# Kernel tuning notes

Hardware: AMD Instinct MI355X
Metric: run time of the kernel (lower is better)

The kernel has to match this reference:

```python
import jax, jax.numpy as jnp
import numpy as np

B, C, H, W = 32, 256, 56, 56
NH, WS, SS = 8, 7, 3
N = WS * WS
EPS = 1e-5


def _rel_pos_index(ws):
    ch, cw = np.meshgrid(np.arange(ws), np.arange(ws), indexing='ij')
    coords = np.stack([ch.reshape(-1), cw.reshape(-1)])  # (2, N)
    rel = coords[:, :, None] - coords[:, None, :]        # (2, N, N)
    rel = rel.transpose(1, 2, 0)
    rel[:, :, 0] += ws - 1
    rel[:, :, 1] += ws - 1
    rel[:, :, 0] *= 2 * ws - 1
    return rel.sum(-1)  # (N, N) int


def _attn_mask(Hh, Ww, ws, ss):
    img = np.zeros((Hh, Ww), dtype=np.float32)
    cnt = 0
    for hs in (slice(0, -ws), slice(-ws, -ss), slice(-ss, None)):
        for wsl in (slice(0, -ws), slice(-ws, -ss), slice(-ss, None)):
            img[hs, wsl] = cnt
            cnt += 1
    mw = img.reshape(Hh // ws, ws, Ww // ws, ws).transpose(0, 2, 1, 3).reshape(-1, ws * ws)
    am = mw[:, None, :] - mw[:, :, None]
    return np.where(am != 0, np.float32(-100.0), np.float32(0.0))  # (nW, N, N)

RPI = _rel_pos_index(WS)
AMASK = _attn_mask(H, W, WS, SS)


def _ln(x, w, b):
    mu = x.mean(-1, keepdims=True)
    var = ((x - mu) ** 2).mean(-1, keepdims=True)
    return (x - mu) * jax.lax.rsqrt(var + EPS) * w + b


def setup_inputs() -> dict:
    key = jax.random.key(0)
    ks = jax.random.split(key, 10)
    s = 0.02
    return {
        'x': jax.random.normal(ks[0], (B, C, H, W), jnp.float32),
        'qkv_w': jax.random.normal(ks[1], (3 * C, C), jnp.float32) * s,
        'q_bias': jnp.zeros((C,), jnp.float32),
        'v_bias': jnp.zeros((C,), jnp.float32),
        'proj_w': jax.random.normal(ks[2], (C, C), jnp.float32) * s,
        'proj_b': jnp.zeros((C,), jnp.float32),
        'rpb_table': jax.random.normal(ks[3], ((2 * WS - 1) * (2 * WS - 1), NH), jnp.float32) * s,
        'norm1_w': jnp.ones((C,), jnp.float32),
        'norm1_b': jnp.zeros((C,), jnp.float32),
        'norm2_w': jnp.ones((C,), jnp.float32),
        'norm2_b': jnp.zeros((C,), jnp.float32),
        'fc1_w': jax.random.normal(ks[4], (4 * C, C), jnp.float32) * s,
        'fc1_b': jnp.zeros((4 * C,), jnp.float32),
        'fc2_w': jax.random.normal(ks[5], (C, 4 * C), jnp.float32) * s,
        'fc2_b': jnp.zeros((C,), jnp.float32),
    }


def reference(x, qkv_w, q_bias, v_bias, proj_w, proj_b, rpb_table,
              norm1_w, norm1_b, norm2_w, norm2_b, fc1_w, fc1_b, fc2_w, fc2_b):
    b = x.shape[0]
    hd = C // NH
    scale = hd ** -0.5
    nWh, nWw = H // WS, W // WS
    nW = nWh * nWw

    # (B,C,H,W) -> (B, L, C)
    xs = x.transpose(0, 2, 3, 1).reshape(b, H * W, C)
    shortcut = xs
    xn = _ln(xs, norm1_w, norm1_b).reshape(b, H, W, C)
    # cyclic shift
    xn = jnp.roll(xn, (-SS, -SS), axis=(1, 2))
    # window partition -> (B*nW, N, C)
    xw = xn.reshape(b, nWh, WS, nWw, WS, C).transpose(0, 1, 3, 2, 4, 5).reshape(b * nW, N, C)

    qkv_bias = jnp.concatenate([q_bias, jnp.zeros_like(v_bias), v_bias])
    qkv = xw @ qkv_w.T + qkv_bias                      # (B_, N, 3C)
    qkv = qkv.reshape(b * nW, N, 3, NH, hd).transpose(2, 0, 3, 1, 4)
    q, k, v = qkv[0], qkv[1], qkv[2]                   # (B_, NH, N, hd)

    attn = jnp.einsum('whnd,whmd->whnm', q * scale, k)  # (B_, NH, N, N)
    bias = rpb_table[RPI.reshape(-1)].reshape(N, N, NH).transpose(2, 0, 1)
    attn = attn + bias[None]
    attn = attn.reshape(b, nW, NH, N, N) + jnp.asarray(AMASK)[None, :, None]
    attn = jax.nn.softmax(attn.reshape(b * nW, NH, N, N), axis=-1)

    out = jnp.einsum('whnm,whmd->whnd', attn, v)        # (B_, NH, N, hd)
    out = out.transpose(0, 2, 1, 3).reshape(b * nW, N, C)
    out = out @ proj_w.T + proj_b

    # window reverse + un-shift
    out = out.reshape(b, nWh, nWw, WS, WS, C).transpose(0, 1, 3, 2, 4, 5).reshape(b, H, W, C)
    out = jnp.roll(out, (SS, SS), axis=(1, 2)).reshape(b, H * W, C)

    xs = shortcut + out
    h = _ln(xs, norm2_w, norm2_b)
    h = jax.nn.relu(h @ fc1_w.T + fc1_b) @ fc2_w.T + fc2_b
    xs = xs + h
    return xs.reshape(b, H, W, C).transpose(0, 3, 1, 2)
```

## Files before the change

kernel.cpp:

```cpp
#include <hip/hip_runtime.h>
#include <math.h>

#define EPS 1e-5f

constexpr int Bc = 32, Cc = 256, Hc = 56, Wc = 56;
constexpr int NHc = 8, HDc = 32, WSc = 7, SSc = 3;
constexpr int NTOK = 49;
constexpr int NWIN = 64;
constexpr int Lc = Hc * Wc;
constexpr int Mrows = Bc * NWIN * NTOK;
constexpr int GIMG = 8;
constexpr int NGRP = Bc / GIMG;
constexpr int ROWS_G = GIMG * Lc;
constexpr int WIN_G = GIMG * NWIN;

typedef short bf16x8 __attribute__((ext_vector_type(8)));
typedef float f32x4 __attribute__((ext_vector_type(4)));
typedef unsigned short u16x8 __attribute__((ext_vector_type(8)));
typedef unsigned short u16x4 __attribute__((ext_vector_type(4)));

__device__ __forceinline__ float bf2f(unsigned short u) {
    return __uint_as_float(((unsigned)u) << 16);
}
__device__ __forceinline__ unsigned short f2bf(float f) {
    unsigned x = __float_as_uint(f);
    return (unsigned short)((x + 0x7fffu + ((x >> 16) & 1u)) >> 16);
}
__device__ __forceinline__ void gload_lds16(const void* g, void* l) {
    __builtin_amdgcn_global_load_lds(
        (const __attribute__((address_space(1))) unsigned int*)g,
        (__attribute__((address_space(3))) unsigned int*)l, 16, 0, 0);
}
__device__ __forceinline__ void inv_swz(int bp, int& row, int& ch) {
    int b2 = ((bp >> 2) ^ (bp >> 4)) & 1;
    int b1_ = ((bp >> 1) ^ (bp >> 3)) & 1;
    int b0 = (bp ^ (bp >> 2) ^ (bp >> 4)) & 1;
    int B = (bp & ~7) | (b2 << 2) | (b1_ << 1) | b0;
    row = B >> 2; ch = B & 3;
}

__global__ __launch_bounds__(256) void k_prep(const float* __restrict__ qkv_w,
                                              const float* __restrict__ proj_w,
                                              const float* __restrict__ w1,
                                              const float* __restrict__ w2,
                                              const float* __restrict__ qb,
                                              const float* __restrict__ vb,
                                              unsigned short* __restrict__ qkv_wb,
                                              unsigned short* __restrict__ proj_wb,
                                              unsigned short* __restrict__ w1t,
                                              unsigned short* __restrict__ w2t,
                                              float* __restrict__ qkvb) {
    int i = blockIdx.x * 256 + threadIdx.x;
    if (i < 768) qkvb[i] = (i < 256) ? qb[i] : ((i < 512) ? 0.f : vb[i - 512]);
    if (i < 196608) qkv_wb[i] = f2bf(qkv_w[i]);
    if (i < 65536)  proj_wb[i] = f2bf(proj_w[i]);
    if (i < 262144) {
        int n1 = i >> 8, k1 = i & 255;
        w1t[((n1 >> 4) * 32 + (k1 >> 3)) * 128 + (n1 & 15) * 8 + (k1 & 7)] = f2bf(w1[i]);
        int n2 = i >> 10, k2 = i & 1023;
        w2t[((k2 >> 6) * 32 + (n2 >> 4) * 2 + ((k2 >> 5) & 1)) * 512 +
            ((k2 >> 3) & 3) * 128 + (n2 & 15) * 8 + (k2 & 7)] = f2bf(w2[i]);
    }
}

__global__ __launch_bounds__(256) void k_ln1_part(const float* __restrict__ x,
                                                  const float* __restrict__ n1w,
                                                  const float* __restrict__ n1b,
                                                  unsigned short* __restrict__ xw,
                                                  unsigned short* __restrict__ xres,
                                                  int b0) {
    __shared__ float s[Cc * 57];
    __shared__ float mu[Wc], rs[Wc];
    int bg = blockIdx.x / Hc, h = blockIdx.x % Hc;
    int b = b0 + bg;
    int t = threadIdx.x;
    const float* xp = x + ((size_t)b * Cc) * Lc + h * Wc;
    for (int idx = t; idx < Cc * Wc; idx += 256) {
        int c = idx / Wc, w = idx % Wc;
        s[c * 57 + w] = xp[(size_t)c * Lc + w];
    }
    __syncthreads();
    int lane = t & 63, wv = t >> 6;
    for (int p = wv; p < Wc; p += 4) {
        float sum = 0.f, sq = 0.f;
        #pragma unroll
        for (int k = 0; k < 4; ++k) {
            float v = s[(lane + 64 * k) * 57 + p];
            sum += v; sq += v * v;
        }
        #pragma unroll
        for (int off = 32; off; off >>= 1) {
            sum += __shfl_xor(sum, off);
            sq  += __shfl_xor(sq, off);
        }
        if (lane == 0) {
            float m = sum / Cc;
            mu[p] = m;
            rs[p] = rsqrtf(sq / Cc - m * m + EPS);
        }
    }
    __syncthreads();
    float wc_ = n1w[t], bc_ = n1b[t];
    int hr = (h + Hc - SSc) % Hc;
    int whh = hr / WSc, th = hr % WSc;
    for (int p = 0; p < Wc; ++p) {
        float raw = s[t * 57 + p];
        xres[((size_t)bg * Lc + h * Wc + p) * Cc + t] = f2bf(raw);
        int wr = (p + Wc - SSc) % Wc;
        int www = wr / WSc, tw = wr % WSc;
        int row = (b * NWIN + whh * 8 + www) * NTOK + th * WSc + tw;
        float v = (raw - mu[p]) * rs[p] * wc_ + bc_;
        xw[(size_t)row * Cc + t] = f2bf(v);
    }
}

__global__ __launch_bounds__(256) void k_gemm_mfma(const unsigned short* __restrict__ A,
                                                   const unsigned short* __restrict__ W,
                                                   const float* __restrict__ bias,
                                                   unsigned short* __restrict__ outb,
                                                   int K, int Nd) {
    __shared__ unsigned short As[128 * 32];
    __shared__ unsigned short Bs[128 * 32];
    int t = threadIdx.x;
    int l = t & 63, w = t >> 6;
    int wm = w & 1, wn = w >> 1;
    int m0 = blockIdx.x * 128, n0 = blockIdx.y * 128;
    int lr = l & 15, lg = l >> 4;

    int row0, ch0, row1, ch1;
    inv_swz(w * 128 + l, row0, ch0);
    inv_swz(w * 128 + 64 + l, row1, ch1);
    const unsigned short* gA0 = A + (size_t)(m0 + row0) * K + ch0 * 8;
    const unsigned short* gA1 = A + (size_t)(m0 + row1) * K + ch1 * 8;
    const unsigned short* gB0 = W + (size_t)(n0 + row0) * K + ch0 * 8;
    const unsigned short* gB1 = W + (size_t)(n0 + row1) * K + ch1 * 8;
    unsigned short* lA0 = &As[(w * 128) * 8];
    unsigned short* lA1 = &As[(w * 128 + 64) * 8];
    unsigned short* lB0 = &Bs[(w * 128) * 8];
    unsigned short* lB1 = &Bs[(w * 128 + 64) * 8];

    f32x4 acc[4][4];
    #pragma unroll
    for (int i = 0; i < 4; ++i)
        #pragma unroll
        for (int j = 0; j < 4; ++j)
            acc[i][j] = (f32x4){0.f, 0.f, 0.f, 0.f};

    for (int kt = 0; kt < K; kt += 32) {
        gload_lds16(gA0 + kt, lA0);
        gload_lds16(gA1 + kt, lA1);
        gload_lds16(gB0 + kt, lB0);
        gload_lds16(gB1 + kt, lB1);
        __syncthreads();
        bf16x8 af[4], bfr[4];
        #pragma unroll
        for (int i = 0; i < 4; ++i) {
            int ra = wm * 64 + i * 16 + lr;
            af[i] = *(bf16x8*)&As[(ra * 32 + lg * 8) ^ ((ra & 7) << 3)];
            int rb = wn * 64 + i * 16 + lr;
            bfr[i] = *(bf16x8*)&Bs[(rb * 32 + lg * 8) ^ ((rb & 7) << 3)];
        }
        #pragma unroll
        for (int i = 0; i < 4; ++i)
            #pragma unroll
            for (int j = 0; j < 4; ++j)
                acc[i][j] = __builtin_amdgcn_mfma_f32_16x16x32_bf16(af[i], bfr[j], acc[i][j], 0, 0, 0);
        __syncthreads();
    }

    float bj[4];
    #pragma unroll
    for (int j = 0; j < 4; ++j) bj[j] = bias[n0 + wn * 64 + j * 16 + lr];
    #pragma unroll
    for (int i = 0; i < 4; ++i)
        #pragma unroll
        for (int j = 0; j < 4; ++j) {
            int col = n0 + wn * 64 + j * 16 + lr;
            #pragma unroll
            for (int r = 0; r < 4; ++r) {
                int row = m0 + wm * 64 + i * 16 + lg * 4 + r;
                outb[(size_t)row * Nd + col] = f2bf(acc[i][j][r] + bj[j]);
            }
        }
}

__global__ __launch_bounds__(256) void k_gemm_proj(const unsigned short* __restrict__ A,
                                                   const unsigned short* __restrict__ W,
                                                   const float* __restrict__ bias,
                                                   const unsigned short* __restrict__ xres,
                                                   unsigned short* __restrict__ xs) {
    __shared__ unsigned short As[128 * 32];
    __shared__ unsigned short Bs[128 * 32];
    constexpr int K = 256;
    int t = threadIdx.x;
    int l = t & 63, w = t >> 6;
    int wm = w & 1, wn = w >> 1;
    int m0 = blockIdx.x * 128, n0 = blockIdx.y * 128;
    int lr = l & 15, lg = l >> 4;

    int row0, ch0, row1, ch1;
    inv_swz(w * 128 + l, row0, ch0);
    inv_swz(w * 128 + 64 + l, row1, ch1);
    const unsigned short* gA0 = A + (size_t)(m0 + row0) * K + ch0 * 8;
    const unsigned short* gA1 = A + (size_t)(m0 + row1) * K + ch1 * 8;
    const unsigned short* gB0 = W + (size_t)(n0 + row0) * K + ch0 * 8;
    const unsigned short* gB1 = W + (size_t)(n0 + row1) * K + ch1 * 8;
    unsigned short* lA0 = &As[(w * 128) * 8];
    unsigned short* lA1 = &As[(w * 128 + 64) * 8];
    unsigned short* lB0 = &Bs[(w * 128) * 8];
    unsigned short* lB1 = &Bs[(w * 128 + 64) * 8];

    f32x4 acc[4][4];
    #pragma unroll
    for (int i = 0; i < 4; ++i)
        #pragma unroll
        for (int j = 0; j < 4; ++j)
            acc[i][j] = (f32x4){0.f, 0.f, 0.f, 0.f};

    for (int kt = 0; kt < K; kt += 32) {
        gload_lds16(gA0 + kt, lA0);
        gload_lds16(gA1 + kt, lA1);
        gload_lds16(gB0 + kt, lB0);
        gload_lds16(gB1 + kt, lB1);
        __syncthreads();
        bf16x8 af[4], bfr[4];
        #pragma unroll
        for (int i = 0; i < 4; ++i) {
            int ra = wm * 64 + i * 16 + lr;
            af[i] = *(bf16x8*)&As[(ra * 32 + lg * 8) ^ ((ra & 7) << 3)];
            int rb = wn * 64 + i * 16 + lr;
            bfr[i] = *(bf16x8*)&Bs[(rb * 32 + lg * 8) ^ ((rb & 7) << 3)];
        }
        #pragma unroll
        for (int i = 0; i < 4; ++i)
            #pragma unroll
            for (int j = 0; j < 4; ++j)
                acc[i][j] = __builtin_amdgcn_mfma_f32_16x16x32_bf16(af[i], bfr[j], acc[i][j], 0, 0, 0);
        __syncthreads();
    }

    float bj[4];
    #pragma unroll
    for (int j = 0; j < 4; ++j) bj[j] = bias[n0 + wn * 64 + j * 16 + lr];
    #pragma unroll
    for (int i = 0; i < 4; ++i)
        #pragma unroll
        for (int j = 0; j < 4; ++j) {
            int col = n0 + wn * 64 + j * 16 + lr;
            #pragma unroll
            for (int r = 0; r < 4; ++r) {
                int row = m0 + wm * 64 + i * 16 + lg * 4 + r;
                int wl = row / NTOK, tok = row - wl * NTOK;
                int bg = wl >> 6, wi = wl & 63;
                int hr = (wi >> 3) * 7 + tok / 7;
                int wr = (wi & 7) * 7 + tok % 7;
                int hh = hr + SSc; if (hh >= Hc) hh -= Hc;
                int ww = wr + SSc; if (ww >= Wc) ww -= Wc;
                size_t didx = ((size_t)bg * Lc + hh * Wc + ww) * Cc + col;
                float res = bf2f(xres[didx]);
                xs[didx] = f2bf(res + acc[i][j][r] + bj[j]);
            }
        }
}

__global__ __launch_bounds__(256) void k_attn(const unsigned short* __restrict__ qkv,
                                              const float* __restrict__ rpb,
                                              unsigned short* __restrict__ outb) {
    __shared__ unsigned short lds[4 * 6144 + 1352];
    unsigned short* rpbs = &lds[4 * 6144];
    int t = threadIdx.x;
    int w = t >> 6, l = t & 63;
    int lr = l & 15, lg = l >> 4;
    unsigned short* wl = &lds[w * 6144];
    unsigned short* Qs = wl;
    unsigned short* Ks = wl + 2048;
    unsigned short* Pm = wl;
    unsigned short* Vt = wl + 4096;

    for (int i = t; i < 1352; i += 256) rpbs[i] = f2bf(rpb[i]);

    int gid = blockIdx.x * 4 + w;
    int b_ = gid >> 3, hh = gid & 7;
    const unsigned short* base = qkv + (size_t)b_ * NTOK * 768 + hh * HDc;

    {
        int j = l;
        u16x8 vq[4], vk[4], vv[4];
        if (j < NTOK) {
            const unsigned short* rp = base + j * 768;
            #pragma unroll
            for (int s = 0; s < 4; ++s) {
                vq[s] = *(const u16x8*)(rp + s * 8);
                vk[s] = *(const u16x8*)(rp + 256 + s * 8);
                vv[s] = *(const u16x8*)(rp + 512 + s * 8);
            }
        } else {
            u16x8 z = {0, 0, 0, 0, 0, 0, 0, 0};
            #pragma unroll
            for (int s = 0; s < 4; ++s) { vq[s] = z; vk[s] = z; vv[s] = z; }
        }
        #pragma unroll
        for (int s = 0; s < 4; ++s) {
            int off = (j * 32 + s * 8) ^ ((j & 7) << 3);
            *(u16x8*)&Qs[off] = vq[s];
            *(u16x8*)&Ks[off] = vk[s];
        }
        #pragma unroll
        for (int s = 0; s < 4; ++s)
            #pragma unroll
            for (int e = 0; e < 8; ++e) {
                int d = s * 8 + e;
                Vt[d * 64 + (j ^ ((d & 7) << 3))] = ((unsigned short*)&vv[s])[e];
            }
    }
    __syncthreads();

    bf16x8 aq[4], bk[4];
    #pragma unroll
    for (int mt = 0; mt < 4; ++mt) {
        int row = mt * 16 + lr;
        int off = (row * 32 + lg * 8) ^ ((row & 7) << 3);
        aq[mt] = *(bf16x8*)&Qs[off];
        bk[mt] = *(bf16x8*)&Ks[off];
    }
    f32x4 sc[4][4];
    #pragma unroll
    for (int mt = 0; mt < 4; ++mt)
        #pragma unroll
        for (int nt = 0; nt < 4; ++nt)
            sc[mt][nt] = __builtin_amdgcn_mfma_f32_16x16x32_bf16(
                aq[mt], bk[nt], (f32x4){0.f, 0.f, 0.f, 0.f}, 0, 0, 0);

    const float scale = 0.17677669529663687f;
    int wi = b_ & 63, wh = wi >> 3, wwc = wi & 7;
    int jh[4], jw[4], ridJ[4];
    #pragma unroll
    for (int nt = 0; nt < 4; ++nt) {
        int j = nt * 16 + lr;
        jh[nt] = j / 7; jw[nt] = j - jh[nt] * 7;
        int gh = wh * 7 + jh[nt], gw = wwc * 7 + jw[nt];
        int rh = gh < 49 ? 0 : (gh < 53 ? 1 : 2);
        int rw = gw < 49 ? 0 : (gw < 53 ? 1 : 2);
        ridJ[nt] = rh * 3 + rw;
    }

    float rowrcp[4][4];
    #pragma unroll
    for (int mt = 0; mt < 4; ++mt) {
        #pragma unroll
        for (int r = 0; r < 4; ++r) {
            int i = mt * 16 + lg * 4 + r;
            int ih = i / 7, iw = i - ih * 7;
            int gh = wh * 7 + ih, gw = wwc * 7 + iw;
            int rhI = gh < 49 ? 0 : (gh < 53 ? 1 : 2);
            int rwI = gw < 49 ? 0 : (gw < 53 ? 1 : 2);
            int ridI = rhI * 3 + rwI;
            bool ivalid = (i < NTOK);
            float vals[4];
            float vmax = -1e30f;
            #pragma unroll
            for (int nt = 0; nt < 4; ++nt) {
                int j = nt * 16 + lr;
                float v = -1e30f;
                if (ivalid && j < NTOK) {
                    int rpi = (ih - jh[nt] + 6) * 13 + (iw - jw[nt] + 6);
                    float bv = bf2f(rpbs[rpi * 8 + hh]);
                    float msk = (ridI == ridJ[nt]) ? 0.f : -100.f;
                    v = sc[mt][nt][r] * scale + bv + msk;
                }
                vals[nt] = v;
                vmax = fmaxf(vmax, v);
            }
            #pragma unroll
            for (int off = 1; off < 16; off <<= 1)
                vmax = fmaxf(vmax, __shfl_xor(vmax, off));
            float s = 0.f;
            unsigned short pb[4];
            #pragma unroll
            for (int nt = 0; nt < 4; ++nt) {
                float e = (vals[nt] > -1e29f) ? __expf(vals[nt] - vmax) : 0.f;
                s += e;
                pb[nt] = f2bf(e);
            }
            #pragma unroll
            for (int off = 1; off < 16; off <<= 1)
                s += __shfl_xor(s, off);
            rowrcp[mt][r] = 1.f / s;
            #pragma unroll
            for (int nt = 0; nt < 4; ++nt) {
                int j = nt * 16 + lr;
                Pm[(i * 64 + j) ^ ((i & 7) << 3)] = pb[nt];
            }
        }
    }

    f32x4 o[4][2];
    #pragma unroll
    for (int mt = 0; mt < 4; ++mt)
        #pragma unroll
        for (int nt = 0; nt < 2; ++nt)
            o[mt][nt] = (f32x4){0.f, 0.f, 0.f, 0.f};
    #pragma unroll
    for (int ks = 0; ks < 2; ++ks) {
        bf16x8 ap[4], bv2[2];
        #pragma unroll
        for (int mt = 0; mt < 4; ++mt) {
            int row = mt * 16 + lr;
            ap[mt] = *(bf16x8*)&Pm[(row * 64 + ks * 32 + lg * 8) ^ ((row & 7) << 3)];
        }
        #pragma unroll
        for (int nt = 0; nt < 2; ++nt) {
            int n = nt * 16 + lr;
            bv2[nt] = *(bf16x8*)&Vt[(n * 64 + ks * 32 + lg * 8) ^ ((n & 7) << 3)];
        }
        #pragma unroll
        for (int mt = 0; mt < 4; ++mt)
            #pragma unroll
            for (int nt = 0; nt < 2; ++nt)
                o[mt][nt] = __builtin_amdgcn_mfma_f32_16x16x32_bf16(ap[mt], bv2[nt], o[mt][nt], 0, 0, 0);
    }

    #pragma unroll
    for (int mt = 0; mt < 4; ++mt)
        #pragma unroll
        for (int r = 0; r < 4; ++r) {
            int i = mt * 16 + lg * 4 + r;
            if (i < NTOK) {
                float rc = rowrcp[mt][r];
                #pragma unroll
                for (int nt = 0; nt < 2; ++nt) {
                    int d = nt * 16 + lr;
                    outb[((size_t)b_ * NTOK + i) * Cc + hh * HDc + d] = f2bf(o[mt][nt][r] * rc);
                }
            }
        }
}

#define HIDX(m, c) (((m) * 64 + (c)) ^ (((m) & 7) << 3))
__global__ __launch_bounds__(512) void k_mlp_fused(const unsigned short* __restrict__ xs,
                                                   const float* __restrict__ n2w,
                                                   const float* __restrict__ n2b,
                                                   const unsigned short* __restrict__ w1t,
                                                   const float* __restrict__ b1,
                                                   const unsigned short* __restrict__ w2t,
                                                   const float* __restrict__ b2,
                                                   float* __restrict__ out) {
    __shared__ unsigned short w1s[16384];
    __shared__ unsigned short w2s[16384];
    __shared__ unsigned short hid[8192];
    int t = threadIdx.x;
    int l = t & 63, w = t >> 6;
    int wm = w >> 1, wn = w & 1;
    int lr = l & 15, lg = l >> 4;
    int m0 = blockIdx.x * 128;

    bf16x8 xf[2][8];
    {
        #pragma unroll
        for (int mf = 0; mf < 2; ++mf) {
            int row = m0 + wm * 32 + mf * 16 + lr;
            const unsigned short* xrow = xs + (size_t)row * Cc;
            u16x8 raw[8];
            float sum = 0.f, sq = 0.f;
            #pragma unroll
            for (int ks = 0; ks < 8; ++ks) {
                raw[ks] = *(const u16x8*)(xrow + ks * 32 + lg * 8);
                #pragma unroll
                for (int e = 0; e < 8; ++e) {
                    float f = bf2f(raw[ks][e]);
                    sum += f; sq += f * f;
                }
            }
            sum += __shfl_xor(sum, 16); sq += __shfl_xor(sq, 16);
            sum += __shfl_xor(sum, 32); sq += __shfl_xor(sq, 32);
            float mu = sum / Cc;
            float rsg = rsqrtf(sq / Cc - mu * mu + EPS);
            #pragma unroll
            for (int ks = 0; ks < 8; ++ks) {
                #pragma unroll
                for (int e = 0; e < 8; ++e) {
                    int c = ks * 32 + lg * 8 + e;
                    float nv = (bf2f(raw[ks][e]) - mu) * rsg * n2w[c] + n2b[c];
                    ((unsigned short*)&xf[mf][ks])[e] = f2bf(nv);
                }
            }
        }
    }

    f32x4 acc2[2][8];
    #pragma unroll
    for (int mf = 0; mf < 2; ++mf)
        #pragma unroll
        for (int nf = 0; nf < 8; ++nf)
            acc2[mf][nf] = (f32x4){0.f, 0.f, 0.f, 0.f};

    u16x8 p1[4], p2[4];
    #pragma unroll
    for (int i = 0; i < 4; ++i) {
        int idx = (i * 512 + t) * 8;
        p1[i] = *(const u16x8*)(w1t + idx);
        p2[i] = *(const u16x8*)(w2t + idx);
    }

    for (int ch = 0; ch < 16; ++ch) {
        #pragma unroll
        for (int i = 0; i < 4; ++i) {
            int idx = (i * 512 + t) * 8;
            *(u16x8*)&w1s[idx] = p1[i];
            *(u16x8*)&w2s[idx] = p2[i];
        }
        __syncthreads();
        if (ch < 15) {
            const unsigned short* n1 = w1t + (ch + 1) * 16384;
            const unsigned short* n2 = w2t + (ch + 1) * 16384;
            #pragma unroll
            for (int i = 0; i < 4; ++i) {
                int idx = (i * 512 + t) * 8;
                p1[i] = *(const u16x8*)(n1 + idx);
                p2[i] = *(const u16x8*)(n2 + idx);
            }
        }
        {
            f32x4 acc1[2][2];
            #pragma unroll
            for (int ht = 0; ht < 2; ++ht)
                #pragma unroll
                for (int mf = 0; mf < 2; ++mf)
                    acc1[ht][mf] = (f32x4){0.f, 0.f, 0.f, 0.f};
            #pragma unroll
            for (int ks = 0; ks < 8; ++ks) {
                bf16x8 wfr[2];
                #pragma unroll
                for (int ht = 0; ht < 2; ++ht)
                    wfr[ht] = *(const bf16x8*)&w1s[(wn * 2 + ht) * 4096 + ks * 512 + l * 8];
                #pragma unroll
                for (int ht = 0; ht < 2; ++ht) {
                    acc1[ht][0] = __builtin_amdgcn_mfma_f32_16x16x32_bf16(wfr[ht], xf[0][ks], acc1[ht][0], 0, 0, 0);
                    acc1[ht][1] = __builtin_amdgcn_mfma_f32_16x16x32_bf16(wfr[ht], xf[1][ks], acc1[ht][1], 0, 0, 0);
                }
            }
            #pragma unroll
            for (int ht = 0; ht < 2; ++ht) {
                float b1v[4];
                #pragma unroll
                for (int r = 0; r < 4; ++r)
                    b1v[r] = b1[ch * 64 + (wn * 2 + ht) * 16 + lg * 4 + r];
                #pragma unroll
                for (int mf = 0; mf < 2; ++mf) {
                    u16x4 pk;
                    #pragma unroll
                    for (int r = 0; r < 4; ++r)
                        pk[r] = f2bf(fmaxf(acc1[ht][mf][r] + b1v[r], 0.f));
                    int m = wm * 32 + mf * 16 + lr;
                    int off = m * 64 + ((((wn * 2 + ht) * 16) + lg * 4) ^ ((m & 7) << 3));
                    *(u16x4*)&hid[off] = pk;
                }
            }
        }
        __syncthreads();
        {
            bf16x8 a[2][2];
            #pragma unroll
            for (int mf = 0; mf < 2; ++mf)
                #pragma unroll
                for (int ks = 0; ks < 2; ++ks) {
                    int m = wm * 32 + mf * 16 + lr;
                    a[mf][ks] = *(const bf16x8*)&hid[HIDX(m, ks * 32 + lg * 8)];
                }
            #pragma unroll
            for (int ks = 0; ks < 2; ++ks)
                #pragma unroll
                for (int nf = 0; nf < 8; ++nf) {
                    int nt = (wn * 128 + nf * 16) >> 4;
                    bf16x8 bfr = *(const bf16x8*)&w2s[(nt * 2 + ks) * 512 + l * 8];
                    acc2[0][nf] = __builtin_amdgcn_mfma_f32_16x16x32_bf16(a[0][ks], bfr, acc2[0][nf], 0, 0, 0);
                    acc2[1][nf] = __builtin_amdgcn_mfma_f32_16x16x32_bf16(a[1][ks], bfr, acc2[1][nf], 0, 0, 0);
                }
        }
        __syncthreads();
    }

    int b0i = m0 / Lc, l0 = m0 % Lc;
    #pragma unroll
    for (int nf = 0; nf < 8; ++nf) {
        int c = wn * 128 + nf * 16 + lr;
        float b2c = b2[c];
        #pragma unroll
        for (int mf = 0; mf < 2; ++mf)
            #pragma unroll
            for (int r = 0; r < 4; ++r) {
                int m = wm * 32 + mf * 16 + lg * 4 + r;
                float res = bf2f(xs[(size_t)(m0 + m) * Cc + c]);
                int lm = l0 + m;
                int bi = b0i + (lm >= Lc);
                if (lm >= Lc) lm -= Lc;
                out[((size_t)bi * Cc + c) * Lc + lm] = acc2[mf][nf][r] + b2c + res;
            }
    }
}

extern "C" void kernel_launch(void* const* d_in, const int* in_sizes, int n_in,
                              void* d_out, int out_size, void* d_ws, size_t ws_size,
                              hipStream_t stream) {
    const float* x      = (const float*)d_in[0];
    const float* qkv_w  = (const float*)d_in[1];
    const float* q_bias = (const float*)d_in[2];
    const float* v_bias = (const float*)d_in[3];
    const float* proj_w = (const float*)d_in[4];
    const float* proj_b = (const float*)d_in[5];
    const float* rpb    = (const float*)d_in[6];
    const float* n1w    = (const float*)d_in[7];
    const float* n1b    = (const float*)d_in[8];
    const float* n2w    = (const float*)d_in[9];
    const float* n2b    = (const float*)d_in[10];
    const float* w1     = (const float*)d_in[11];
    const float* b1     = (const float*)d_in[12];
    const float* w2     = (const float*)d_in[13];
    const float* b2     = (const float*)d_in[14];

    char* ws = (char*)d_ws;
    const size_t SZ_BF16 = (size_t)Mrows * Cc * 2;
    unsigned short* xw      = (unsigned short*)ws;
    float*          qkvb    = (float*)(ws + SZ_BF16);
    unsigned short* qkv_wb  = (unsigned short*)(ws + SZ_BF16 + 3072);
    unsigned short* proj_wb = qkv_wb + 196608;
    unsigned short* w1t     = proj_wb + 65536;
    unsigned short* w2t     = w1t + 262144;

    unsigned short* qkv_s  = (unsigned short*)d_out;
    unsigned short* attn_s = qkv_s + (size_t)ROWS_G * 768;
    unsigned short* xres_s = attn_s + (size_t)ROWS_G * Cc;

    k_prep<<<1024, 256, 0, stream>>>(qkv_w, proj_w, w1, w2, q_bias, v_bias,
                                     qkv_wb, proj_wb, w1t, w2t, qkvb);

    for (int g = 0; g < NGRP; ++g) {
        unsigned short* xw_g = xw + (size_t)g * ROWS_G * Cc;
        k_ln1_part<<<GIMG * Hc, 256, 0, stream>>>(x, n1w, n1b, xw, xres_s, g * GIMG);
        k_gemm_mfma<<<dim3(ROWS_G / 128, 768 / 128), 256, 0, stream>>>(
            xw_g, qkv_wb, qkvb, qkv_s, 256, 768);
        k_attn<<<WIN_G * NHc / 4, 256, 0, stream>>>(qkv_s, rpb, attn_s);
        k_gemm_proj<<<dim3(ROWS_G / 128, 2), 256, 0, stream>>>(
            attn_s, proj_wb, proj_b, xres_s, xw_g);
    }

    k_mlp_fused<<<Mrows / 128, 512, 0, stream>>>(xw, n2w, n2b, w1t, b1, w2t, b2,
                                                 (float*)d_out);
}
```

Before: 567.2 us.

## Write attention output in place over qkv, double group size, stream fc2 weights

The attention kernel now writes its output in place into the Q slot of the qkv scratch buffer, and the projection GEMM reads A with a row stride of 768. This drops the separate attention buffer, so the d_out scratch can hold groups of 16 images instead of 8, halving the number of per-group launches. The fused MLP no longer stages fc2 weights in LDS and reads them straight from global/L2 per fragment. That cuts LDS use, which may improve occupancy, but adds global load latency inside the MFMA loop. The in-place write is safe only if each wave has finished reading its Q slice before writing, which holds because each (window, head) pair touches only its own Q columns.

```diff
diff --git a/kernel.cpp b/kernel.cpp
--- a/kernel.cpp
+++ b/kernel.cpp
@@ -9,7 +9,7 @@
 constexpr int NWIN = 64;
 constexpr int Lc = Hc * Wc;
 constexpr int Mrows = Bc * NWIN * NTOK;
-constexpr int GIMG = 8;
+constexpr int GIMG = 16;
 constexpr int NGRP = Bc / GIMG;
 constexpr int ROWS_G = GIMG * Lc;
 constexpr int WIN_G = GIMG * NWIN;
@@ -192,6 +192,7 @@
     __shared__ unsigned short As[128 * 32];
     __shared__ unsigned short Bs[128 * 32];
     constexpr int K = 256;
+    constexpr int LDA = 768;
     int t = threadIdx.x;
     int l = t & 63, w = t >> 6;
     int wm = w & 1, wn = w >> 1;
@@ -201,8 +202,8 @@
     int row0, ch0, row1, ch1;
     inv_swz(w * 128 + l, row0, ch0);
     inv_swz(w * 128 + 64 + l, row1, ch1);
-    const unsigned short* gA0 = A + (size_t)(m0 + row0) * K + ch0 * 8;
-    const unsigned short* gA1 = A + (size_t)(m0 + row1) * K + ch1 * 8;
+    const unsigned short* gA0 = A + (size_t)(m0 + row0) * LDA + ch0 * 8;
+    const unsigned short* gA1 = A + (size_t)(m0 + row1) * LDA + ch1 * 8;
     const unsigned short* gB0 = W + (size_t)(n0 + row0) * K + ch0 * 8;
     const unsigned short* gB1 = W + (size_t)(n0 + row1) * K + ch1 * 8;
     unsigned short* lA0 = &As[(w * 128) * 8];
@@ -263,9 +264,8 @@
         }
 }
 
-__global__ __launch_bounds__(256) void k_attn(const unsigned short* __restrict__ qkv,
-                                              const float* __restrict__ rpb,
-                                              unsigned short* __restrict__ outb) {
+__global__ __launch_bounds__(256) void k_attn(unsigned short* __restrict__ qkv,
+                                              const float* __restrict__ rpb) {
     __shared__ unsigned short lds[4 * 6144 + 1352];
     unsigned short* rpbs = &lds[4 * 6144];
     int t = threadIdx.x;
@@ -281,7 +281,7 @@
 
     int gid = blockIdx.x * 4 + w;
     int b_ = gid >> 3, hh = gid & 7;
-    const unsigned short* base = qkv + (size_t)b_ * NTOK * 768 + hh * HDc;
+    unsigned short* base = qkv + (size_t)b_ * NTOK * 768 + hh * HDc;
 
     {
         int j = l;
@@ -430,7 +430,7 @@
                 #pragma unroll
                 for (int nt = 0; nt < 2; ++nt) {
                     int d = nt * 16 + lr;
-                    outb[((size_t)b_ * NTOK + i) * Cc + hh * HDc + d] = f2bf(o[mt][nt][r] * rc);
+                    qkv[((size_t)b_ * NTOK + i) * 768 + hh * HDc + d] = f2bf(o[mt][nt][r] * rc);
                 }
             }
         }
@@ -446,7 +446,6 @@
                                                    const float* __restrict__ b2,
                                                    float* __restrict__ out) {
     __shared__ unsigned short w1s[16384];
-    __shared__ unsigned short w2s[16384];
     __shared__ unsigned short hid[8192];
     int t = threadIdx.x;
     int l = t & 63, w = t >> 6;
@@ -494,31 +493,21 @@
         for (int nf = 0; nf < 8; ++nf)
             acc2[mf][nf] = (f32x4){0.f, 0.f, 0.f, 0.f};
 
-    u16x8 p1[4], p2[4];
-    #pragma unroll
-    for (int i = 0; i < 4; ++i) {
-        int idx = (i * 512 + t) * 8;
-        p1[i] = *(const u16x8*)(w1t + idx);
-        p2[i] = *(const u16x8*)(w2t + idx);
-    }
+    u16x8 p1[4];
+    #pragma unroll
+    for (int i = 0; i < 4; ++i)
+        p1[i] = *(const u16x8*)(w1t + (i * 512 + t) * 8);
 
     for (int ch = 0; ch < 16; ++ch) {
         #pragma unroll
-        for (int i = 0; i < 4; ++i) {
-            int idx = (i * 512 + t) * 8;
-            *(u16x8*)&w1s[idx] = p1[i];
-            *(u16x8*)&w2s[idx] = p2[i];
-        }
+        for (int i = 0; i < 4; ++i)
+            *(u16x8*)&w1s[(i * 512 + t) * 8] = p1[i];
         __syncthreads();
         if (ch < 15) {
             const unsigned short* n1 = w1t + (ch + 1) * 16384;
-            const unsigned short* n2 = w2t + (ch + 1) * 16384;
-            #pragma unroll
-            for (int i = 0; i < 4; ++i) {
-                int idx = (i * 512 + t) * 8;
-                p1[i] = *(const u16x8*)(n1 + idx);
-                p2[i] = *(const u16x8*)(n2 + idx);
-            }
+            #pragma unroll
+            for (int i = 0; i < 4; ++i)
+                p1[i] = *(const u16x8*)(n1 + (i * 512 + t) * 8);
         }
         {
             f32x4 acc1[2][2];
@@ -567,12 +556,13 @@
                     int m = wm * 32 + mf * 16 + lr;
                     a[mf][ks] = *(const bf16x8*)&hid[HIDX(m, ks * 32 + lg * 8)];
                 }
+            const unsigned short* w2c = w2t + ch * 16384;
             #pragma unroll
             for (int ks = 0; ks < 2; ++ks)
                 #pragma unroll
                 for (int nf = 0; nf < 8; ++nf) {
-                    int nt = (wn * 128 + nf * 16) >> 4;
-                    bf16x8 bfr = *(const bf16x8*)&w2s[(nt * 2 + ks) * 512 + l * 8];
+                    int nt = wn * 8 + nf;
+                    bf16x8 bfr = *(const bf16x8*)&w2c[(nt * 2 + ks) * 512 + l * 8];
                     acc2[0][nf] = __builtin_amdgcn_mfma_f32_16x16x32_bf16(a[0][ks], bfr, acc2[0][nf], 0, 0, 0);
                     acc2[1][nf] = __builtin_amdgcn_mfma_f32_16x16x32_bf16(a[1][ks], bfr, acc2[1][nf], 0, 0, 0);
                 }
@@ -628,8 +618,7 @@
     unsigned short* w2t     = w1t + 262144;
 
     unsigned short* qkv_s  = (unsigned short*)d_out;
-    unsigned short* attn_s = qkv_s + (size_t)ROWS_G * 768;
-    unsigned short* xres_s = attn_s + (size_t)ROWS_G * Cc;
+    unsigned short* xres_s = qkv_s + (size_t)ROWS_G * 768;
 
     k_prep<<<1024, 256, 0, stream>>>(qkv_w, proj_w, w1, w2, q_bias, v_bias,
                                      qkv_wb, proj_wb, w1t, w2t, qkvb);
@@ -639,9 +628,9 @@
         k_ln1_part<<<GIMG * Hc, 256, 0, stream>>>(x, n1w, n1b, xw, xres_s, g * GIMG);
         k_gemm_mfma<<<dim3(ROWS_G / 128, 768 / 128), 256, 0, stream>>>(
             xw_g, qkv_wb, qkvb, qkv_s, 256, 768);
-        k_attn<<<WIN_G * NHc / 4, 256, 0, stream>>>(qkv_s, rpb, attn_s);
+        k_attn<<<WIN_G * NHc / 4, 256, 0, stream>>>(qkv_s, rpb);
         k_gemm_proj<<<dim3(ROWS_G / 128, 2), 256, 0, stream>>>(
-            attn_s, proj_wb, proj_b, xres_s, xw_g);
+            qkv_s, proj_wb, proj_b, xres_s, xw_g);
     }
 
     k_mlp_fused<<<Mrows / 128, 512, 0, stream>>>(xw, n2w, n2b, w1t, b1, w2t, b2,
```

Result: slower. 616.6 us (+8.7%).
